# Performance work log

Measured on AMD Instinct MI355X. Metric: run time of the kernel, lower is better.

The kernel has to match this reference:

```python
import jax, jax.numpy as jnp
import numpy as np

D_MODEL = 1024
H = 16
D_HEAD = D_MODEL // H  # 64


def setup_inputs() -> dict:
    key = jax.random.key(0)
    ks = jax.random.split(key, 11)
    B, L = 4, 1024
    s = 0.02
    return {
        "Q": jax.random.normal(ks[0], (B, L, D_MODEL), jnp.float32),
        "K": jax.random.normal(ks[1], (B, L, D_MODEL), jnp.float32),
        "V": jax.random.normal(ks[2], (B, L, D_MODEL), jnp.float32),
        # per-head Dense weights stacked on a leading head axis (Keras Dense: y = x @ W + b)
        "Wq": jax.random.normal(ks[3], (H, D_MODEL, D_HEAD), jnp.float32) * s,
        "bq": jnp.zeros((H, D_HEAD), jnp.float32),
        "Wk": jax.random.normal(ks[4], (H, D_MODEL, D_HEAD), jnp.float32) * s,
        "bk": jnp.zeros((H, D_HEAD), jnp.float32),
        "Wv": jax.random.normal(ks[5], (H, D_MODEL, D_HEAD), jnp.float32) * s,
        "bv": jnp.zeros((H, D_HEAD), jnp.float32),
        "Wo": jax.random.normal(ks[6], (D_MODEL, D_MODEL), jnp.float32) * s,
        "bo": jnp.zeros((D_MODEL,), jnp.float32),
    }


def reference(Q, K, V, Wq, bq, Wk, bk, Wv, bv, Wo, bo):
    # per-head projections, vectorized over heads: [B, H, L, Dh]
    q = jnp.einsum("bld,hde->bhle", Q, Wq) + bq[None, :, None, :]
    k = jnp.einsum("bld,hde->bhle", K, Wk) + bk[None, :, None, :]
    v = jnp.einsum("bld,hde->bhle", V, Wv) + bv[None, :, None, :]
    # scaled dot-product attention scores: [B, H, Lq, Lk]
    scores = jnp.einsum("bhqe,bhke->bhqk", q, k) / jnp.sqrt(jnp.asarray(D_HEAD, q.dtype))
    attn = jax.nn.softmax(scores, axis=-1)
    out_h = jnp.einsum("bhqk,bhke->bhqe", attn, v)  # [B, H, Lq, Dh]
    # concat heads along feature dim (matches tf.concat(heads, axis=2))
    B, Hh, Lq, Dh = out_h.shape
    concat = out_h.transpose(0, 2, 1, 3).reshape(B, Lq, Hh * Dh)
    output = concat @ Wo + bo
    # tf.stack(heads_attention) -> [H, B, Lq, Lk]
    attention = attn.transpose(1, 0, 2, 3)
    return output, attention
```

## Files before the change

### kernel.cpp

```cpp
#include <hip/hip_runtime.h>
#include <stdint.h>

#define DEVI __device__ __forceinline__
typedef unsigned short u16;
typedef __attribute__((ext_vector_type(8))) short s16x8;
typedef __attribute__((ext_vector_type(4))) float f32x4;

typedef __attribute__((address_space(1))) void as1_void;
typedef __attribute__((address_space(3))) void as3_void;

DEVI u16 f2b(float f){
  union { float f; uint32_t u; } x; x.f = f;
  return (u16)((x.u + 0x7fffu + ((x.u >> 16) & 1u)) >> 16);
}
DEVI float b2f(u16 u){
  union { uint32_t u; float f; } x; x.u = ((uint32_t)u) << 16;
  return x.f;
}
DEVI void gload16(const void* g, void* l){
  __builtin_amdgcn_global_load_lds((as1_void*)g, (as3_void*)l, 16, 0, 0);
}
DEVI f32x4 MFMA(s16x8 a, s16x8 b, f32x4 c){
  return __builtin_amdgcn_mfma_f32_16x16x32_bf16(a, b, c, 0, 0, 0);
}

__global__ __launch_bounds__(256)
void k_prep(const float* __restrict__ Q, const float* __restrict__ Kc,
            const float* __restrict__ V,
            u16* __restrict__ Qb, u16* __restrict__ Kb, u16* __restrict__ Vb,
            const float* __restrict__ Wq, const float* __restrict__ Wk,
            const float* __restrict__ Wv, const float* __restrict__ Wo,
            u16* __restrict__ WqT, u16* __restrict__ WkT,
            u16* __restrict__ WvT, u16* __restrict__ WoT){
  __shared__ float t[64][65];
  const int bid = blockIdx.x, tid = threadIdx.x;
  if(bid < 12288){
    int tno = bid >> 12;
    int blk = bid & 4095;
    const float* s = (tno == 0) ? Q : (tno == 1) ? Kc : V;
    u16* d = (tno == 0) ? Qb : (tno == 1) ? Kb : Vb;
    int i = (blk * 256 + tid) * 4;
    float4 v = *(const float4*)(s + i);
    ushort4 o;
    o.x = f2b(v.x); o.y = f2b(v.y); o.z = f2b(v.z); o.w = f2b(v.w);
    *(ushort4*)(d + i) = o;
  } else {
    int j = bid - 12288;
    const float* src; u16* dst; int C, r0, c0;
    if(j < 768){
      int tno = j >> 8, rem = j & 255, head = rem >> 4, rt = rem & 15;
      src = ((tno == 0) ? Wq : (tno == 1) ? Wk : Wv) + head * 65536;
      dst = ((tno == 0) ? WqT : (tno == 1) ? WkT : WvT) + head * 65536;
      C = 64; r0 = rt * 64; c0 = 0;
    } else {
      int j2 = j - 768;
      src = Wo; dst = WoT; C = 1024;
      r0 = (j2 & 15) * 64; c0 = (j2 >> 4) * 64;
    }
    int tx = tid & 63, ty = tid >> 6;
    #pragma unroll
    for(int i2 = 0; i2 < 64; i2 += 4)
      t[ty + i2][tx] = src[(size_t)(r0 + ty + i2) * C + c0 + tx];
    __syncthreads();
    #pragma unroll
    for(int i2 = 0; i2 < 64; i2 += 4)
      dst[(size_t)(c0 + ty + i2) * 1024 + r0 + tx] = f2b(t[tx][ty + i2]);
  }
}

template<int BM, int BK>
DEVI void gemm_core(int mode, const u16* __restrict__ A, const u16* __restrict__ Bt,
                    const float* __restrict__ bias, void* __restrict__ Cp,
                    int m0, int n0, u16* sAb, u16* sBb){
  const int tid = threadIdx.x, w = tid >> 6, l = tid & 63;
  const int wr = w >> 1, wc = w & 1;
  constexpr int MI = BM / 32;
  constexpr int KK = BK / 32;
  constexpr int CPR = BK / 8;
  constexpr int CPT_A = BM * BK / 2048;
  constexpr int CPT_B = 128 * BK / 2048;
  constexpr int RB = 2 * BK;
  f32x4 acc[MI][4];
  #pragma unroll
  for(int a = 0; a < MI; a++)
    #pragma unroll
    for(int b = 0; b < 4; b++) acc[a][b] = (f32x4){0.f, 0.f, 0.f, 0.f};

  const int NT = 1024 / BK;
  auto STAGE = [&](int buf, int t){
    #pragma unroll
    for(int s2 = 0; s2 < CPT_A; s2++){
      int c = s2 * 256 + tid;
      int r = c / CPR, ch = (c % CPR) ^ (r & (CPR - 1));
      gload16((const char*)A + ((size_t)(m0 + r) * 1024 + t * BK) * 2 + ch * 16,
              (char*)sAb + (size_t)buf * BM * RB + c * 16);
    }
    #pragma unroll
    for(int s2 = 0; s2 < CPT_B; s2++){
      int c = s2 * 256 + tid;
      int r = c / CPR, ch = (c % CPR) ^ (r & (CPR - 1));
      gload16((const char*)Bt + ((size_t)(n0 + r) * 1024 + t * BK) * 2 + ch * 16,
              (char*)sBb + (size_t)buf * 128 * RB + c * 16);
    }
  };
  STAGE(0, 0);
  __syncthreads();
  for(int t = 0; t < NT; t++){
    const int cur = t & 1;
    if(t + 1 < NT) STAGE(cur ^ 1, t + 1);
    const char* pa = (const char*)sAb + (size_t)cur * BM * RB;
    const char* pb = (const char*)sBb + (size_t)cur * 128 * RB;
    s16x8 af[MI][KK], bf[4][KK];
    #pragma unroll
    for(int mi = 0; mi < MI; mi++){
      int r = (BM / 2) * wr + 16 * mi + (l & 15);
      #pragma unroll
      for(int kk = 0; kk < KK; kk++)
        af[mi][kk] = *(const s16x8*)(pa + r * RB +
                     ((kk * 64 + 16 * (l >> 4)) ^ ((r & (CPR - 1)) << 4)));
    }
    #pragma unroll
    for(int ni = 0; ni < 4; ni++){
      int r = 64 * wc + 16 * ni + (l & 15);
      #pragma unroll
      for(int kk = 0; kk < KK; kk++)
        bf[ni][kk] = *(const s16x8*)(pb + r * RB +
                     ((kk * 64 + 16 * (l >> 4)) ^ ((r & (CPR - 1)) << 4)));
    }
    #pragma unroll
    for(int kk = 0; kk < KK; kk++)
      #pragma unroll
      for(int mi = 0; mi < MI; mi++)
        #pragma unroll
        for(int ni = 0; ni < 4; ni++)
          acc[mi][ni] = MFMA(af[mi][kk], bf[ni][kk], acc[mi][ni]);
    __syncthreads();
  }
  #pragma unroll
  for(int mi = 0; mi < MI; mi++){
    #pragma unroll
    for(int ni = 0; ni < 4; ni++){
      #pragma unroll
      for(int i = 0; i < 4; i++){
        int gr = m0 + (BM / 2) * wr + 16 * mi + 4 * (l >> 4) + i;
        int gc = n0 + 64 * wc + 16 * ni + (l & 15);
        float v = acc[mi][ni][i];
        if(mode == 0){
          ((u16*)Cp)[(size_t)gr * 1024 + gc] = f2b(v + bias[gc]);
        } else if(mode == 1){
          ((u16*)Cp)[((size_t)(gc >> 10) << 20) + ((size_t)gr << 10) + (gc & 1023)] =
              f2b(v + bias[gr]);
        } else {
          ((float*)Cp)[(size_t)gr * 1024 + gc] = v + bias[gc];
        }
      }
    }
  }
}

__global__ __launch_bounds__(256, 3)
void k_proj(const u16* __restrict__ Qb, const u16* __restrict__ Kb,
            const u16* __restrict__ Vb,
            const u16* __restrict__ WqT, const u16* __restrict__ WkT,
            const u16* __restrict__ WvT,
            const float* __restrict__ bq, const float* __restrict__ bk,
            const float* __restrict__ bv,
            u16* __restrict__ q_ws, u16* __restrict__ k_ws, u16* __restrict__ vT_ws){
  __shared__ u16 sA[2][128 * 32];
  __shared__ u16 sB[2][128 * 32];
  const int raw = blockIdx.x;
  const int bid = (raw & 7) * 96 + (raw >> 3);
  if(bid < 256){
    gemm_core<128, 32>(0, Qb, WqT, bq, q_ws, (bid >> 3) * 128, (bid & 7) * 128,
                       &sA[0][0], &sB[0][0]);
  } else if(bid < 512){
    int b2 = bid - 256;
    gemm_core<128, 32>(0, Kb, WkT, bk, k_ws, (b2 >> 3) * 128, (b2 & 7) * 128,
                       &sA[0][0], &sB[0][0]);
  } else {
    int b2 = bid - 512;
    gemm_core<128, 32>(1, WvT, Vb, bv, vT_ws, (b2 >> 5) * 128, (b2 & 31) * 128,
                       &sA[0][0], &sB[0][0]);
  }
}

__global__ __launch_bounds__(256)
void k_final(const u16* __restrict__ A, const u16* __restrict__ Bt,
             const float* __restrict__ bias, float* __restrict__ C){
  __shared__ u16 sA[2][64 * 64];
  __shared__ u16 sB[2][128 * 64];
  const int raw = blockIdx.x;
  const int bid = (raw & 7) * 64 + (raw >> 3);
  gemm_core<64, 64>(2, A, Bt, bias, C, (bid >> 3) * 64, (bid & 7) * 128,
                    &sA[0][0], &sB[0][0]);
}

__global__ __launch_bounds__(256, 4)
void k_attn(const u16* __restrict__ qws, const u16* __restrict__ kws,
            const u16* __restrict__ vws, float* __restrict__ attn,
            u16* __restrict__ concat){
  __shared__ u16 k_s[2][64 * 64];
  __shared__ u16 v_s[2][64 * 64];
  __shared__ u16 p_s[64 * 64];
  const int tid = threadIdx.x, w = tid >> 6, l = tid & 63;
  const int bx = blockIdx.x;
  const int bh = bx & 63, qb = bx >> 6, b = bh >> 4, h = bh & 15;
  const char* qg = (const char*)qws + ((size_t)(b * 1024 + qb * 64) * 1024 + h * 64) * 2;
  const char* kg = (const char*)kws + ((size_t)(b * 1024) * 1024 + h * 64) * 2;
  const char* vg = (const char*)vws + ((size_t)b * 1048576 + (size_t)h * 64 * 1024) * 2;
  float* ao = attn + (size_t)((h * 4 + b) * 1024 + qb * 64) * 1024;
  u16* cw = concat + (size_t)(b * 1024 + qb * 64) * 1024 + h * 64;

  auto STAGEK = [&](int buf, int kt){
    #pragma unroll
    for(int rd = 0; rd < 2; rd++){
      int c = rd * 256 + tid;
      int r = c >> 3, ch = c & 7;
      gload16(kg + (size_t)(kt * 64 + r) * 2048 + ((ch ^ (r & 7)) * 16),
              (char*)k_s[buf] + c * 16);
    }
  };
  auto STAGEV = [&](int buf, int kt){
    #pragma unroll
    for(int rd = 0; rd < 2; rd++){
      int c = rd * 256 + tid;
      int e = c >> 3, ch = c & 7;
      gload16(vg + (size_t)e * 2048 + kt * 128 + ((ch ^ (e & 7)) * 16),
              (char*)v_s[buf] + c * 16);
    }
  };

  s16x8 af0, af1;
  {
    int rq = 16 * w + (l & 15);
    af0 = *(const s16x8*)(qg + (size_t)rq * 2048 + (l >> 4) * 16);
    af1 = *(const s16x8*)(qg + (size_t)rq * 2048 + 64 + (l >> 4) * 16);
  }

  const float KS = 0.18033688011112042f;
  float rs[4] = {0.f, 0.f, 0.f, 0.f};

  STAGEK(0, 0);
  __syncthreads();
  for(int kt = 0; kt < 16; kt++){
    const int cur = kt & 1;
    if(kt + 1 < 16) STAGEK(cur ^ 1, kt + 1);
    #pragma unroll
    for(int f = 0; f < 4; f++){
      int r = 16 * f + (l & 15);
      s16x8 b0 = *(const s16x8*)((const char*)k_s[cur] + r * 128 + ((16 * (l >> 4)) ^ ((r & 7) << 4)));
      s16x8 b1 = *(const s16x8*)((const char*)k_s[cur] + r * 128 + ((64 + 16 * (l >> 4)) ^ ((r & 7) << 4)));
      f32x4 sf = (f32x4){0.f, 0.f, 0.f, 0.f};
      sf = MFMA(af0, b0, sf);
      sf = MFMA(af1, b1, sf);
      #pragma unroll
      for(int i = 0; i < 4; i++) rs[i] += exp2f(sf[i] * KS);
    }
    __syncthreads();
  }
  #pragma unroll
  for(int i = 0; i < 4; i++){
    #pragma unroll
    for(int m = 1; m < 16; m <<= 1) rs[i] += __shfl_xor(rs[i], m, 64);
  }
  float inv[4];
  #pragma unroll
  for(int i = 0; i < 4; i++) inv[i] = 1.0f / rs[i];

  f32x4 oacc[4];
  #pragma unroll
  for(int fe = 0; fe < 4; fe++) oacc[fe] = (f32x4){0.f, 0.f, 0.f, 0.f};

  STAGEK(0, 0);
  STAGEV(0, 0);
  __syncthreads();
  for(int kt = 0; kt < 16; kt++){
    const int cur = kt & 1;
    if(kt + 1 < 16){ STAGEK(cur ^ 1, kt + 1); STAGEV(cur ^ 1, kt + 1); }
    f32x4 sf[4];
    #pragma unroll
    for(int f = 0; f < 4; f++){
      int r = 16 * f + (l & 15);
      s16x8 b0 = *(const s16x8*)((const char*)k_s[cur] + r * 128 + ((16 * (l >> 4)) ^ ((r & 7) << 4)));
      s16x8 b1 = *(const s16x8*)((const char*)k_s[cur] + r * 128 + ((64 + 16 * (l >> 4)) ^ ((r & 7) << 4)));
      sf[f] = (f32x4){0.f, 0.f, 0.f, 0.f};
      sf[f] = MFMA(af0, b0, sf[f]);
      sf[f] = MFMA(af1, b1, sf[f]);
    }
    #pragma unroll
    for(int f = 0; f < 4; f++){
      #pragma unroll
      for(int i = 0; i < 4; i++){
        float p = exp2f(sf[f][i] * KS) * inv[i];
        int rr = 16 * w + 4 * (l >> 4) + i;
        int cc = 16 * f + (l & 15);
        *(u16*)((char*)p_s + rr * 128 + ((cc * 2) ^ ((rr & 7) << 4))) = f2b(p);
      }
    }
    #pragma unroll
    for(int kc = 0; kc < 2; kc++){
      int rp = 16 * w + (l & 15);
      s16x8 pa = *(const s16x8*)((const char*)p_s + rp * 128 +
                  ((kc * 64 + 16 * (l >> 4)) ^ ((rp & 7) << 4)));
      #pragma unroll
      for(int fe = 0; fe < 4; fe++){
        int e = 16 * fe + (l & 15);
        s16x8 bv = *(const s16x8*)((const char*)v_s[cur] + e * 128 +
                    ((kc * 64 + 16 * (l >> 4)) ^ ((e & 7) << 4)));
        oacc[fe] = MFMA(pa, bv, oacc[fe]);
      }
    }
    #pragma unroll
    for(int it = 0; it < 4; it++){
      int row = 16 * w + 4 * it + (l >> 4);
      uint2 pv = *(const uint2*)((const char*)p_s + row * 128 +
                                 ((8 * (l & 15)) ^ ((row & 7) << 4)));
      f32x4 o;
      o[0] = b2f((u16)(pv.x & 0xffffu));
      o[1] = b2f((u16)(pv.x >> 16));
      o[2] = b2f((u16)(pv.y & 0xffffu));
      o[3] = b2f((u16)(pv.y >> 16));
      *(f32x4*)(ao + (size_t)row * 1024 + kt * 64 + (l & 15) * 4) = o;
    }
    __syncthreads();
  }
  #pragma unroll
  for(int fe = 0; fe < 4; fe++){
    #pragma unroll
    for(int i = 0; i < 4; i++){
      int qi = 16 * w + 4 * (l >> 4) + i;
      cw[(size_t)qi * 1024 + 16 * fe + (l & 15)] = f2b(oacc[fe][i]);
    }
  }
}

extern "C" void kernel_launch(void* const* d_in, const int* in_sizes, int n_in,
                              void* d_out, int out_size, void* d_ws, size_t ws_size,
                              hipStream_t stream){
  const float* Q  = (const float*)d_in[0];
  const float* Kc = (const float*)d_in[1];
  const float* V  = (const float*)d_in[2];
  const float* Wq = (const float*)d_in[3];
  const float* bq = (const float*)d_in[4];
  const float* Wk = (const float*)d_in[5];
  const float* bk = (const float*)d_in[6];
  const float* Wv = (const float*)d_in[7];
  const float* bv = (const float*)d_in[8];
  const float* Wo = (const float*)d_in[9];
  const float* bo = (const float*)d_in[10];
  float* out = (float*)d_out;

  char* ws = (char*)d_ws;
  u16* q_ws      = (u16*)(ws + 0);
  u16* k_ws      = (u16*)(ws + 8388608);
  u16* vT_ws     = (u16*)(ws + 16777216);
  u16* concat_ws = (u16*)(ws + 25165824);
  u16* WqT = (u16*)(ws + 33554432);
  u16* WkT = (u16*)(ws + 35651584);
  u16* WvT = (u16*)(ws + 37748736);
  u16* WoT = (u16*)(ws + 39845888);

  u16* Qb = (u16*)((char*)d_out + 16777216);
  u16* Kb = (u16*)((char*)d_out + 25165824);
  u16* Vb = (u16*)((char*)d_out + 33554432);
  float* attn = out + 4194304;

  k_prep<<<13312, 256, 0, stream>>>(Q, Kc, V, Qb, Kb, Vb,
                                    Wq, Wk, Wv, Wo, WqT, WkT, WvT, WoT);
  k_proj<<<768, 256, 0, stream>>>(Qb, Kb, Vb, WqT, WkT, WvT, bq, bk, bv,
                                  q_ws, k_ws, vT_ws);
  k_attn<<<1024, 256, 0, stream>>>(q_ws, k_ws, vT_ws, attn, concat_ws);
  k_final<<<512, 256, 0, stream>>>(concat_ws, WoT, bo, out);
}
```

Before: 158.4 us.

## Cache unnormalized exp scores in registers to skip second QK^T pass

The first pass now saves the bf16-packed exp(score) values in a 128-register array, fully unrolled. The second pass reuses them instead of reloading K and recomputing the QK^T MFMAs and exps, and only streams V. This removes half the K traffic and MFMA work. The attention matrix is now written straight from registers as scalar fp32 stores rather than vectorized 16-byte stores read back from LDS. The extra register pressure forces launch bounds from 4 to 2 waves per SIMD, lowering occupancy. The global attention writes become narrower and may coalesce less well.

Measured after the change: 211.9 us. 1.34x slower.

```diff
diff --git a/kernel.cpp b/kernel.cpp
--- a/kernel.cpp
+++ b/kernel.cpp
@@ -195,7 +195,7 @@
                     &sA[0][0], &sB[0][0]);
 }
 
-__global__ __launch_bounds__(256, 4)
+__global__ __launch_bounds__(256, 2)
 void k_attn(const u16* __restrict__ qws, const u16* __restrict__ kws,
             const u16* __restrict__ vws, float* __restrict__ attn,
             u16* __restrict__ concat){
@@ -239,9 +239,11 @@
 
   const float KS = 0.18033688011112042f;
   float rs[4] = {0.f, 0.f, 0.f, 0.f};
+  uint32_t preg[16][8];
 
   STAGEK(0, 0);
   __syncthreads();
+  #pragma unroll
   for(int kt = 0; kt < 16; kt++){
     const int cur = kt & 1;
     if(kt + 1 < 16) STAGEK(cur ^ 1, kt + 1);
@@ -254,7 +256,13 @@
       sf = MFMA(af0, b0, sf);
       sf = MFMA(af1, b1, sf);
       #pragma unroll
-      for(int i = 0; i < 4; i++) rs[i] += exp2f(sf[i] * KS);
+      for(int ip = 0; ip < 2; ip++){
+        float e0 = exp2f(sf[2 * ip] * KS);
+        float e1 = exp2f(sf[2 * ip + 1] * KS);
+        rs[2 * ip] += e0;
+        rs[2 * ip + 1] += e1;
+        preg[kt][f * 2 + ip] = (uint32_t)f2b(e0) | ((uint32_t)f2b(e1) << 16);
+      }
     }
     __syncthreads();
   }
@@ -271,30 +279,26 @@
   #pragma unroll
   for(int fe = 0; fe < 4; fe++) oacc[fe] = (f32x4){0.f, 0.f, 0.f, 0.f};
 
-  STAGEK(0, 0);
   STAGEV(0, 0);
   __syncthreads();
+  #pragma unroll
   for(int kt = 0; kt < 16; kt++){
     const int cur = kt & 1;
-    if(kt + 1 < 16){ STAGEK(cur ^ 1, kt + 1); STAGEV(cur ^ 1, kt + 1); }
-    f32x4 sf[4];
+    if(kt + 1 < 16) STAGEV(cur ^ 1, kt + 1);
     #pragma unroll
     for(int f = 0; f < 4; f++){
-      int r = 16 * f + (l & 15);
-      s16x8 b0 = *(const s16x8*)((const char*)k_s[cur] + r * 128 + ((16 * (l >> 4)) ^ ((r & 7) << 4)));
-      s16x8 b1 = *(const s16x8*)((const char*)k_s[cur] + r * 128 + ((64 + 16 * (l >> 4)) ^ ((r & 7) << 4)));
-      sf[f] = (f32x4){0.f, 0.f, 0.f, 0.f};
-      sf[f] = MFMA(af0, b0, sf[f]);
-      sf[f] = MFMA(af1, b1, sf[f]);
-    }
-    #pragma unroll
-    for(int f = 0; f < 4; f++){
-      #pragma unroll
-      for(int i = 0; i < 4; i++){
-        float p = exp2f(sf[f][i] * KS) * inv[i];
-        int rr = 16 * w + 4 * (l >> 4) + i;
-        int cc = 16 * f + (l & 15);
-        *(u16*)((char*)p_s + rr * 128 + ((cc * 2) ^ ((rr & 7) << 4))) = f2b(p);
+      #pragma unroll
+      for(int ip = 0; ip < 2; ip++){
+        uint32_t pk = preg[kt][f * 2 + ip];
+        #pragma unroll
+        for(int s = 0; s < 2; s++){
+          int i = 2 * ip + s;
+          float p = b2f((u16)((pk >> (16 * s)) & 0xffffu)) * inv[i];
+          int rr = 16 * w + 4 * (l >> 4) + i;
+          int cc = 16 * f + (l & 15);
+          *(u16*)((char*)p_s + rr * 128 + ((cc * 2) ^ ((rr & 7) << 4))) = f2b(p);
+          ao[(size_t)rr * 1024 + kt * 64 + cc] = p;
+        }
       }
     }
     #pragma unroll
@@ -309,18 +313,6 @@
                     ((kc * 64 + 16 * (l >> 4)) ^ ((e & 7) << 4)));
         oacc[fe] = MFMA(pa, bv, oacc[fe]);
       }
-    }
-    #pragma unroll
-    for(int it = 0; it < 4; it++){
-      int row = 16 * w + 4 * it + (l >> 4);
-      uint2 pv = *(const uint2*)((const char*)p_s + row * 128 +
-                                 ((8 * (l & 15)) ^ ((row & 7) << 4)));
-      f32x4 o;
-      o[0] = b2f((u16)(pv.x & 0xffffu));
-      o[1] = b2f((u16)(pv.x >> 16));
-      o[2] = b2f((u16)(pv.y & 0xffffu));
-      o[3] = b2f((u16)(pv.y >> 16));
-      *(f32x4*)(ao + (size_t)row * 1024 + kt * 64 + (l & 15) * 4) = o;
     }
     __syncthreads();
   }
```

## Fuse fp32-to-bf16 activation conversion into projection GEMM loads

Applied to the files above, without the earlier changes.

Drops the separate pass that converted the Q, K and V activations to bf16 in the output buffer. The projection GEMM now reads the fp32 activations directly into registers, converts them, and writes bf16 into shared memory using a register-staged double buffer, with the stores placed after the MFMAs. This removes a full write and re-read of the bf16 activations, but the fp32 operand is read at twice the byte count and goes through registers instead of the direct global-to-LDS load, which raises register pressure.

Result: slower. 187.3 us (+18.2%).

```diff
diff --git a/kernel.cpp b/kernel.cpp
--- a/kernel.cpp
+++ b/kernel.cpp
@@ -4,6 +4,7 @@
 #define DEVI __device__ __forceinline__
 typedef unsigned short u16;
 typedef __attribute__((ext_vector_type(8))) short s16x8;
+typedef __attribute__((ext_vector_type(8))) unsigned short u16x8;
 typedef __attribute__((ext_vector_type(4))) float f32x4;
 
 typedef __attribute__((address_space(1))) void as1_void;
@@ -25,51 +26,35 @@
 }
 
 __global__ __launch_bounds__(256)
-void k_prep(const float* __restrict__ Q, const float* __restrict__ Kc,
-            const float* __restrict__ V,
-            u16* __restrict__ Qb, u16* __restrict__ Kb, u16* __restrict__ Vb,
-            const float* __restrict__ Wq, const float* __restrict__ Wk,
+void k_prep(const float* __restrict__ Wq, const float* __restrict__ Wk,
             const float* __restrict__ Wv, const float* __restrict__ Wo,
             u16* __restrict__ WqT, u16* __restrict__ WkT,
             u16* __restrict__ WvT, u16* __restrict__ WoT){
   __shared__ float t[64][65];
-  const int bid = blockIdx.x, tid = threadIdx.x;
-  if(bid < 12288){
-    int tno = bid >> 12;
-    int blk = bid & 4095;
-    const float* s = (tno == 0) ? Q : (tno == 1) ? Kc : V;
-    u16* d = (tno == 0) ? Qb : (tno == 1) ? Kb : Vb;
-    int i = (blk * 256 + tid) * 4;
-    float4 v = *(const float4*)(s + i);
-    ushort4 o;
-    o.x = f2b(v.x); o.y = f2b(v.y); o.z = f2b(v.z); o.w = f2b(v.w);
-    *(ushort4*)(d + i) = o;
+  const int j = blockIdx.x, tid = threadIdx.x;
+  const float* src; u16* dst; int C, r0, c0;
+  if(j < 768){
+    int tno = j >> 8, rem = j & 255, head = rem >> 4, rt = rem & 15;
+    src = ((tno == 0) ? Wq : (tno == 1) ? Wk : Wv) + head * 65536;
+    dst = ((tno == 0) ? WqT : (tno == 1) ? WkT : WvT) + head * 65536;
+    C = 64; r0 = rt * 64; c0 = 0;
   } else {
-    int j = bid - 12288;
-    const float* src; u16* dst; int C, r0, c0;
-    if(j < 768){
-      int tno = j >> 8, rem = j & 255, head = rem >> 4, rt = rem & 15;
-      src = ((tno == 0) ? Wq : (tno == 1) ? Wk : Wv) + head * 65536;
-      dst = ((tno == 0) ? WqT : (tno == 1) ? WkT : WvT) + head * 65536;
-      C = 64; r0 = rt * 64; c0 = 0;
-    } else {
-      int j2 = j - 768;
-      src = Wo; dst = WoT; C = 1024;
-      r0 = (j2 & 15) * 64; c0 = (j2 >> 4) * 64;
-    }
-    int tx = tid & 63, ty = tid >> 6;
-    #pragma unroll
-    for(int i2 = 0; i2 < 64; i2 += 4)
-      t[ty + i2][tx] = src[(size_t)(r0 + ty + i2) * C + c0 + tx];
-    __syncthreads();
-    #pragma unroll
-    for(int i2 = 0; i2 < 64; i2 += 4)
-      dst[(size_t)(c0 + ty + i2) * 1024 + r0 + tx] = f2b(t[tx][ty + i2]);
-  }
-}
-
-template<int BM, int BK>
-DEVI void gemm_core(int mode, const u16* __restrict__ A, const u16* __restrict__ Bt,
+    int j2 = j - 768;
+    src = Wo; dst = WoT; C = 1024;
+    r0 = (j2 & 15) * 64; c0 = (j2 >> 4) * 64;
+  }
+  int tx = tid & 63, ty = tid >> 6;
+  #pragma unroll
+  for(int i2 = 0; i2 < 64; i2 += 4)
+    t[ty + i2][tx] = src[(size_t)(r0 + ty + i2) * C + c0 + tx];
+  __syncthreads();
+  #pragma unroll
+  for(int i2 = 0; i2 < 64; i2 += 4)
+    dst[(size_t)(c0 + ty + i2) * 1024 + r0 + tx] = f2b(t[tx][ty + i2]);
+}
+
+template<int BM, int BK, int OMODE, bool AF32, bool BF32>
+DEVI void gemm_core(const void* __restrict__ Ap, const void* __restrict__ Btp,
                     const float* __restrict__ bias, void* __restrict__ Cp,
                     int m0, int n0, u16* sAb, u16* sBb){
   const int tid = threadIdx.x, w = tid >> 6, l = tid & 63;
@@ -86,28 +71,92 @@
     #pragma unroll
     for(int b = 0; b < 4; b++) acc[a][b] = (f32x4){0.f, 0.f, 0.f, 0.f};
 
+  float4 la[AF32 ? CPT_A : 1][2];
+  float4 lb[BF32 ? CPT_B : 1][2];
+
+  auto LOADA = [&](int t){
+    if(AF32){
+      #pragma unroll
+      for(int s2 = 0; s2 < CPT_A; s2++){
+        int c = s2 * 256 + tid;
+        int r = c / CPR, ch = (c % CPR) ^ (r & (CPR - 1));
+        const float* src = (const float*)Ap + (size_t)(m0 + r) * 1024 + t * BK + ch * 8;
+        la[s2][0] = *(const float4*)src;
+        la[s2][1] = *(const float4*)(src + 4);
+      }
+    }
+  };
+  auto LOADB = [&](int t){
+    if(BF32){
+      #pragma unroll
+      for(int s2 = 0; s2 < CPT_B; s2++){
+        int c = s2 * 256 + tid;
+        int r = c / CPR, ch = (c % CPR) ^ (r & (CPR - 1));
+        const float* src = (const float*)Btp + (size_t)(n0 + r) * 1024 + t * BK + ch * 8;
+        lb[s2][0] = *(const float4*)src;
+        lb[s2][1] = *(const float4*)(src + 4);
+      }
+    }
+  };
+  auto DMAA = [&](int buf, int t){
+    if(!AF32){
+      #pragma unroll
+      for(int s2 = 0; s2 < CPT_A; s2++){
+        int c = s2 * 256 + tid;
+        int r = c / CPR, ch = (c % CPR) ^ (r & (CPR - 1));
+        gload16((const char*)Ap + ((size_t)(m0 + r) * 1024 + t * BK) * 2 + ch * 16,
+                (char*)sAb + (size_t)buf * BM * RB + c * 16);
+      }
+    }
+  };
+  auto DMAB = [&](int buf, int t){
+    if(!BF32){
+      #pragma unroll
+      for(int s2 = 0; s2 < CPT_B; s2++){
+        int c = s2 * 256 + tid;
+        int r = c / CPR, ch = (c % CPR) ^ (r & (CPR - 1));
+        gload16((const char*)Btp + ((size_t)(n0 + r) * 1024 + t * BK) * 2 + ch * 16,
+                (char*)sBb + (size_t)buf * 128 * RB + c * 16);
+      }
+    }
+  };
+  auto WRITEA = [&](int buf){
+    if(AF32){
+      #pragma unroll
+      for(int s2 = 0; s2 < CPT_A; s2++){
+        int c = s2 * 256 + tid;
+        u16x8 o;
+        #pragma unroll
+        for(int jj = 0; jj < 4; jj++){
+          o[jj]     = f2b(la[s2][0][jj]);
+          o[4 + jj] = f2b(la[s2][1][jj]);
+        }
+        *(u16x8*)((char*)sAb + (size_t)buf * BM * RB + c * 16) = o;
+      }
+    }
+  };
+  auto WRITEB = [&](int buf){
+    if(BF32){
+      #pragma unroll
+      for(int s2 = 0; s2 < CPT_B; s2++){
+        int c = s2 * 256 + tid;
+        u16x8 o;
+        #pragma unroll
+        for(int jj = 0; jj < 4; jj++){
+          o[jj]     = f2b(lb[s2][0][jj]);
+          o[4 + jj] = f2b(lb[s2][1][jj]);
+        }
+        *(u16x8*)((char*)sBb + (size_t)buf * 128 * RB + c * 16) = o;
+      }
+    }
+  };
+
   const int NT = 1024 / BK;
-  auto STAGE = [&](int buf, int t){
-    #pragma unroll
-    for(int s2 = 0; s2 < CPT_A; s2++){
-      int c = s2 * 256 + tid;
-      int r = c / CPR, ch = (c % CPR) ^ (r & (CPR - 1));
-      gload16((const char*)A + ((size_t)(m0 + r) * 1024 + t * BK) * 2 + ch * 16,
-              (char*)sAb + (size_t)buf * BM * RB + c * 16);
-    }
-    #pragma unroll
-    for(int s2 = 0; s2 < CPT_B; s2++){
-      int c = s2 * 256 + tid;
-      int r = c / CPR, ch = (c % CPR) ^ (r & (CPR - 1));
-      gload16((const char*)Bt + ((size_t)(n0 + r) * 1024 + t * BK) * 2 + ch * 16,
-              (char*)sBb + (size_t)buf * 128 * RB + c * 16);
-    }
-  };
-  STAGE(0, 0);
+  LOADA(0); LOADB(0); DMAA(0, 0); DMAB(0, 0); WRITEA(0); WRITEB(0);
   __syncthreads();
   for(int t = 0; t < NT; t++){
     const int cur = t & 1;
-    if(t + 1 < NT) STAGE(cur ^ 1, t + 1);
+    if(t + 1 < NT){ LOADA(t + 1); LOADB(t + 1); DMAA(cur ^ 1, t + 1); DMAB(cur ^ 1, t + 1); }
     const char* pa = (const char*)sAb + (size_t)cur * BM * RB;
     const char* pb = (const char*)sBb + (size_t)cur * 128 * RB;
     s16x8 af[MI][KK], bf[4][KK];
@@ -134,6 +183,7 @@
         #pragma unroll
         for(int ni = 0; ni < 4; ni++)
           acc[mi][ni] = MFMA(af[mi][kk], bf[ni][kk], acc[mi][ni]);
+    if(t + 1 < NT){ WRITEA(cur ^ 1); WRITEB(cur ^ 1); }
     __syncthreads();
   }
   #pragma unroll
@@ -145,9 +195,9 @@
         int gr = m0 + (BM / 2) * wr + 16 * mi + 4 * (l >> 4) + i;
         int gc = n0 + 64 * wc + 16 * ni + (l & 15);
         float v = acc[mi][ni][i];
-        if(mode == 0){
+        if(OMODE == 0){
           ((u16*)Cp)[(size_t)gr * 1024 + gc] = f2b(v + bias[gc]);
-        } else if(mode == 1){
+        } else if(OMODE == 1){
           ((u16*)Cp)[((size_t)(gc >> 10) << 20) + ((size_t)gr << 10) + (gc & 1023)] =
               f2b(v + bias[gr]);
         } else {
@@ -159,8 +209,8 @@
 }
 
 __global__ __launch_bounds__(256, 3)
-void k_proj(const u16* __restrict__ Qb, const u16* __restrict__ Kb,
-            const u16* __restrict__ Vb,
+void k_proj(const float* __restrict__ Q, const float* __restrict__ Kc,
+            const float* __restrict__ V,
             const u16* __restrict__ WqT, const u16* __restrict__ WkT,
             const u16* __restrict__ WvT,
             const float* __restrict__ bq, const float* __restrict__ bk,
@@ -171,16 +221,16 @@
   const int raw = blockIdx.x;
   const int bid = (raw & 7) * 96 + (raw >> 3);
   if(bid < 256){
-    gemm_core<128, 32>(0, Qb, WqT, bq, q_ws, (bid >> 3) * 128, (bid & 7) * 128,
-                       &sA[0][0], &sB[0][0]);
+    gemm_core<128, 32, 0, true, false>(Q, WqT, bq, q_ws,
+        (bid >> 3) * 128, (bid & 7) * 128, &sA[0][0], &sB[0][0]);
   } else if(bid < 512){
     int b2 = bid - 256;
-    gemm_core<128, 32>(0, Kb, WkT, bk, k_ws, (b2 >> 3) * 128, (b2 & 7) * 128,
-                       &sA[0][0], &sB[0][0]);
+    gemm_core<128, 32, 0, true, false>(Kc, WkT, bk, k_ws,
+        (b2 >> 3) * 128, (b2 & 7) * 128, &sA[0][0], &sB[0][0]);
   } else {
     int b2 = bid - 512;
-    gemm_core<128, 32>(1, WvT, Vb, bv, vT_ws, (b2 >> 5) * 128, (b2 & 31) * 128,
-                       &sA[0][0], &sB[0][0]);
+    gemm_core<128, 32, 1, false, true>(WvT, V, bv, vT_ws,
+        (b2 >> 5) * 128, (b2 & 31) * 128, &sA[0][0], &sB[0][0]);
   }
 }
 
@@ -191,8 +241,8 @@
   __shared__ u16 sB[2][128 * 64];
   const int raw = blockIdx.x;
   const int bid = (raw & 7) * 64 + (raw >> 3);
-  gemm_core<64, 64>(2, A, Bt, bias, C, (bid >> 3) * 64, (bid & 7) * 128,
-                    &sA[0][0], &sB[0][0]);
+  gemm_core<64, 64, 2, false, false>(A, Bt, bias, C,
+      (bid >> 3) * 64, (bid & 7) * 128, &sA[0][0], &sB[0][0]);
 }
 
 __global__ __launch_bounds__(256, 4)
@@ -360,14 +410,10 @@
   u16* WvT = (u16*)(ws + 37748736);
   u16* WoT = (u16*)(ws + 39845888);
 
-  u16* Qb = (u16*)((char*)d_out + 16777216);
-  u16* Kb = (u16*)((char*)d_out + 25165824);
-  u16* Vb = (u16*)((char*)d_out + 33554432);
   float* attn = out + 4194304;
 
-  k_prep<<<13312, 256, 0, stream>>>(Q, Kc, V, Qb, Kb, Vb,
-                                    Wq, Wk, Wv, Wo, WqT, WkT, WvT, WoT);
-  k_proj<<<768, 256, 0, stream>>>(Qb, Kb, Vb, WqT, WkT, WvT, bq, bk, bv,
+  k_prep<<<1024, 256, 0, stream>>>(Wq, Wk, Wv, Wo, WqT, WkT, WvT, WoT);
+  k_proj<<<768, 256, 0, stream>>>(Q, Kc, V, WqT, WkT, WvT, bq, bk, bv,
                                   q_ws, k_ws, vT_ws);
   k_attn<<<1024, 256, 0, stream>>>(q_ws, k_ws, vT_ws, attn, concat_ws);
   k_final<<<512, 256, 0, stream>>>(concat_ws, WoT, bo, out);
```

## Load K and V fragments directly from global memory, dropping LDS staging

Applied to the files above, without the earlier changes.

The attention kernel no longer double-buffers K and V tiles through shared memory with async global-to-LDS loads. Each wave now reads its MFMA B-operand fragments straight from global memory into registers, and the per-tile block barriers are removed. The aim is to cut LDS usage and synchronisation so waves run independently and more blocks fit per CU. The cost is that all four waves fetch the same K/V data redundantly, and the per-lane reads are short strided 16-byte accesses that depend on cache hits.

After: 263.5 us. 1.66x slower.

```diff
diff --git a/kernel.cpp b/kernel.cpp
--- a/kernel.cpp
+++ b/kernel.cpp
@@ -199,8 +199,6 @@
 void k_attn(const u16* __restrict__ qws, const u16* __restrict__ kws,
             const u16* __restrict__ vws, float* __restrict__ attn,
             u16* __restrict__ concat){
-  __shared__ u16 k_s[2][64 * 64];
-  __shared__ u16 v_s[2][64 * 64];
   __shared__ u16 p_s[64 * 64];
   const int tid = threadIdx.x, w = tid >> 6, l = tid & 63;
   const int bx = blockIdx.x;
@@ -211,25 +209,6 @@
   float* ao = attn + (size_t)((h * 4 + b) * 1024 + qb * 64) * 1024;
   u16* cw = concat + (size_t)(b * 1024 + qb * 64) * 1024 + h * 64;
 
-  auto STAGEK = [&](int buf, int kt){
-    #pragma unroll
-    for(int rd = 0; rd < 2; rd++){
-      int c = rd * 256 + tid;
-      int r = c >> 3, ch = c & 7;
-      gload16(kg + (size_t)(kt * 64 + r) * 2048 + ((ch ^ (r & 7)) * 16),
-              (char*)k_s[buf] + c * 16);
-    }
-  };
-  auto STAGEV = [&](int buf, int kt){
-    #pragma unroll
-    for(int rd = 0; rd < 2; rd++){
-      int c = rd * 256 + tid;
-      int e = c >> 3, ch = c & 7;
-      gload16(vg + (size_t)e * 2048 + kt * 128 + ((ch ^ (e & 7)) * 16),
-              (char*)v_s[buf] + c * 16);
-    }
-  };
-
   s16x8 af0, af1;
   {
     int rq = 16 * w + (l & 15);
@@ -240,23 +219,18 @@
   const float KS = 0.18033688011112042f;
   float rs[4] = {0.f, 0.f, 0.f, 0.f};
 
-  STAGEK(0, 0);
-  __syncthreads();
   for(int kt = 0; kt < 16; kt++){
-    const int cur = kt & 1;
-    if(kt + 1 < 16) STAGEK(cur ^ 1, kt + 1);
     #pragma unroll
     for(int f = 0; f < 4; f++){
-      int r = 16 * f + (l & 15);
-      s16x8 b0 = *(const s16x8*)((const char*)k_s[cur] + r * 128 + ((16 * (l >> 4)) ^ ((r & 7) << 4)));
-      s16x8 b1 = *(const s16x8*)((const char*)k_s[cur] + r * 128 + ((64 + 16 * (l >> 4)) ^ ((r & 7) << 4)));
+      const char* kr = kg + (size_t)(kt * 64 + 16 * f + (l & 15)) * 2048 + (l >> 4) * 16;
+      s16x8 b0 = *(const s16x8*)(kr);
+      s16x8 b1 = *(const s16x8*)(kr + 64);
       f32x4 sf = (f32x4){0.f, 0.f, 0.f, 0.f};
       sf = MFMA(af0, b0, sf);
       sf = MFMA(af1, b1, sf);
       #pragma unroll
       for(int i = 0; i < 4; i++) rs[i] += exp2f(sf[i] * KS);
     }
-    __syncthreads();
   }
   #pragma unroll
   for(int i = 0; i < 4; i++){
@@ -271,18 +245,13 @@
   #pragma unroll
   for(int fe = 0; fe < 4; fe++) oacc[fe] = (f32x4){0.f, 0.f, 0.f, 0.f};
 
-  STAGEK(0, 0);
-  STAGEV(0, 0);
-  __syncthreads();
   for(int kt = 0; kt < 16; kt++){
-    const int cur = kt & 1;
-    if(kt + 1 < 16){ STAGEK(cur ^ 1, kt + 1); STAGEV(cur ^ 1, kt + 1); }
     f32x4 sf[4];
     #pragma unroll
     for(int f = 0; f < 4; f++){
-      int r = 16 * f + (l & 15);
-      s16x8 b0 = *(const s16x8*)((const char*)k_s[cur] + r * 128 + ((16 * (l >> 4)) ^ ((r & 7) << 4)));
-      s16x8 b1 = *(const s16x8*)((const char*)k_s[cur] + r * 128 + ((64 + 16 * (l >> 4)) ^ ((r & 7) << 4)));
+      const char* kr = kg + (size_t)(kt * 64 + 16 * f + (l & 15)) * 2048 + (l >> 4) * 16;
+      s16x8 b0 = *(const s16x8*)(kr);
+      s16x8 b1 = *(const s16x8*)(kr + 64);
       sf[f] = (f32x4){0.f, 0.f, 0.f, 0.f};
       sf[f] = MFMA(af0, b0, sf[f]);
       sf[f] = MFMA(af1, b1, sf[f]);
@@ -305,8 +274,8 @@
       #pragma unroll
       for(int fe = 0; fe < 4; fe++){
         int e = 16 * fe + (l & 15);
-        s16x8 bv = *(const s16x8*)((const char*)v_s[cur] + e * 128 +
-                    ((kc * 64 + 16 * (l >> 4)) ^ ((e & 7) << 4)));
+        s16x8 bv = *(const s16x8*)(vg + (size_t)e * 2048 + kt * 128 + kc * 64 +
+                                   (l >> 4) * 16);
         oacc[fe] = MFMA(pa, bv, oacc[fe]);
       }
     }
@@ -322,7 +291,6 @@
       o[3] = b2f((u16)(pv.y >> 16));
       *(f32x4*)(ao + (size_t)row * 1024 + kt * 64 + (l & 15) * 4) = o;
     }
-    __syncthreads();
   }
   #pragma unroll
   for(int fe = 0; fe < 4; fe++){
```
